# Kernel optimization log

Hardware: AMD Instinct MI355X
Metric: run time of the kernel (lower is better)

## Reference

```python
import jax, jax.numpy as jnp
import numpy as np


def setup_inputs() -> dict:
    key = jax.random.key(0)
    k1, k2 = jax.random.split(key)
    n, c, H, W = 8, 16, 512, 512
    pred = jax.random.normal(k1, (n, c, H, W), dtype=jnp.float32)
    target = jax.random.randint(k2, (n, H, W), 0, c, dtype=jnp.int64)
    weights = jnp.ones((n, 1, H, W), dtype=jnp.float32)  # ignored by the module
    return {"pred": pred, "target": target, "weights": weights}


def reference(pred, target, weights):
    # pred: [n,c,H,W] logits; target: [n,H,W] int class ids; weights arg is ignored
    n, c, H, W = pred.shape
    # Global (whole-batch) per-class pixel counts -> inverse-frequency weights.
    counts = jnp.zeros((c,), dtype=pred.dtype).at[target.reshape(-1)].add(1.0)
    w_class = jnp.where(counts > 0, 1.0 / (counts * c), 0.0)  # [c]
    w = w_class[target]  # [n,H,W] per-pixel weight (constant w.r.t. pred)
    # log-softmax gathered at target class per pixel
    logp = jax.nn.log_softmax(pred, axis=1)  # [n,c,H,W]
    lp_t = jnp.take_along_axis(logp, target[:, None, :, :], axis=1)[:, 0]  # [n,H,W]
    num = (lp_t * w).reshape(n, -1).sum(axis=1)  # [n]
    den = w.reshape(n, -1).sum(axis=1)           # [n]
    return -(num / den).mean()
```

## Files before the change

### kernel.cpp

```cpp
#include <hip/hip_runtime.h>

#define NIMG 8
#define NCLS 16
#define HW      262144
#define PXB     2048
#define NBLK    1024
#define GROUPS  2

__global__ __launch_bounds__(256) void dwce_main(const float* __restrict__ pred,
                                                 const int* __restrict__ tgt,
                                                 float* __restrict__ partials) {
    __shared__ float s_bin[32];
    const int tid = threadIdx.x;
    if (tid < 32) s_bin[tid] = 0.0f;
    __syncthreads();

    const int b = blockIdx.x;
    const long long px0 = (long long)b * PXB;
    const int n_img = (int)(px0 >> 18);
    const int hw0   = (int)(px0 & (HW - 1));
    const float* base = pred + (size_t)n_img * NCLS * HW + hw0;

    const int w    = tid >> 6;
    const int lane = tid & 63;
    int idx[GROUPS];
#pragma unroll
    for (int g = 0; g < GROUPS; ++g)
        idx[g] = w * (GROUPS * 256) + g * 256 + lane * 4;

    int4 t[GROUPS];
#pragma unroll
    for (int g = 0; g < GROUPS; ++g)
        t[g] = *(const int4*)(tgt + px0 + idx[g]);

    float4 m[GROUPS], s[GROUPS], xt[GROUPS];
#pragma unroll
    for (int g = 0; g < GROUPS; ++g) {
        m[g]  = make_float4(-3.0e38f, -3.0e38f, -3.0e38f, -3.0e38f);
        s[g]  = make_float4(0.f, 0.f, 0.f, 0.f);
        xt[g] = make_float4(0.f, 0.f, 0.f, 0.f);
    }

#pragma unroll 2
    for (int c = 0; c < NCLS; ++c) {
        const float* cb = base + (size_t)c * HW;
#pragma unroll
        for (int g = 0; g < GROUPS; ++g) {
            const float4 v = *(const float4*)(cb + idx[g]);
            float4 mn;
            mn.x = fmaxf(m[g].x, v.x);
            mn.y = fmaxf(m[g].y, v.y);
            mn.z = fmaxf(m[g].z, v.z);
            mn.w = fmaxf(m[g].w, v.w);
            s[g].x = s[g].x * __expf(m[g].x - mn.x) + __expf(v.x - mn.x);
            s[g].y = s[g].y * __expf(m[g].y - mn.y) + __expf(v.y - mn.y);
            s[g].z = s[g].z * __expf(m[g].z - mn.z) + __expf(v.z - mn.z);
            s[g].w = s[g].w * __expf(m[g].w - mn.w) + __expf(v.w - mn.w);
            m[g] = mn;
            if (t[g].x == c) xt[g].x = v.x;
            if (t[g].y == c) xt[g].y = v.y;
            if (t[g].z == c) xt[g].z = v.z;
            if (t[g].w == c) xt[g].w = v.w;
        }
    }

#pragma unroll
    for (int g = 0; g < GROUPS; ++g) {
        const float lp0 = xt[g].x - (m[g].x + __logf(s[g].x));
        const float lp1 = xt[g].y - (m[g].y + __logf(s[g].y));
        const float lp2 = xt[g].z - (m[g].z + __logf(s[g].z));
        const float lp3 = xt[g].w - (m[g].w + __logf(s[g].w));
        atomicAdd(&s_bin[t[g].x], lp0);
        atomicAdd(&s_bin[t[g].y], lp1);
        atomicAdd(&s_bin[t[g].z], lp2);
        atomicAdd(&s_bin[t[g].w], lp3);
        atomicAdd(&s_bin[16 + t[g].x], 1.0f);
        atomicAdd(&s_bin[16 + t[g].y], 1.0f);
        atomicAdd(&s_bin[16 + t[g].z], 1.0f);
        atomicAdd(&s_bin[16 + t[g].w], 1.0f);
    }

    __syncthreads();
    if (tid < 32)
        partials[(size_t)tid * NBLK + b] = s_bin[tid];
}

__global__ __launch_bounds__(256) void dwce_final(const float* __restrict__ ws,
                                                  float* __restrict__ out) {
    __shared__ float tot[32][NIMG];
    __shared__ float wcl[NCLS];
    __shared__ float ratio[NIMG];
    const int tid = threadIdx.x;
    const int c = tid >> 3;
    const int n = tid & 7;

    const float4* p = (const float4*)(ws + (size_t)c * NBLK + n * 128);
    float4 a = make_float4(0.f, 0.f, 0.f, 0.f);
#pragma unroll 8
    for (int k = 0; k < 32; ++k) {
        float4 q = p[k];
        a.x += q.x; a.y += q.y; a.z += q.z; a.w += q.w;
    }
    tot[c][n] = (a.x + a.y) + (a.z + a.w);
    __syncthreads();

    if (tid < NCLS) {
        float g = 0.f;
#pragma unroll
        for (int i = 0; i < NIMG; ++i) g += tot[NCLS + tid][i];
        wcl[tid] = (g > 0.f) ? 1.0f / (g * (float)NCLS) : 0.0f;
    }
    __syncthreads();
    if (tid < NIMG) {
        float num = 0.f, den = 0.f;
#pragma unroll
        for (int c2 = 0; c2 < NCLS; ++c2) {
            num += tot[c2][tid] * wcl[c2];
            den += tot[NCLS + c2][tid] * wcl[c2];
        }
        ratio[tid] = num / den;
    }
    __syncthreads();
    if (tid == 0) {
        float r = 0.f;
#pragma unroll
        for (int i = 0; i < NIMG; ++i) r += ratio[i];
        out[0] = -r * (1.0f / (float)NIMG);
    }
}

extern "C" void kernel_launch(void* const* d_in, const int* in_sizes, int n_in,
                              void* d_out, int out_size, void* d_ws, size_t ws_size,
                              hipStream_t stream) {
    const float* pred = (const float*)d_in[0];
    const int*   tgt  = (const int*)d_in[1];
    float* out = (float*)d_out;
    float* ws  = (float*)d_ws;

    dwce_main<<<NBLK, 256, 0, stream>>>(pred, tgt, ws);
    dwce_final<<<1, 256, 0, stream>>>(ws, out);
}
```

Baseline: 223.0 us.

## Stage logits in LDS via global_load_lds and use two-pass softmax

```diff
diff --git a/kernel.cpp b/kernel.cpp
--- a/kernel.cpp
+++ b/kernel.cpp
@@ -1,19 +1,26 @@
 #include <hip/hip_runtime.h>
+#include <stdint.h>
 
 #define NIMG 8
 #define NCLS 16
-#define HW      262144
-#define PXB     2048
-#define NBLK    1024
-#define GROUPS  2
+#define HW   262144
+#define PXB  1024
+#define NBLK 2048
+
+__device__ __forceinline__ void g2lds16(const float* g, float* l) {
+    __builtin_amdgcn_global_load_lds(
+        (const __attribute__((address_space(1))) unsigned int*)g,
+        (__attribute__((address_space(3))) unsigned int*)l,
+        16, 0, 0);
+}
 
 __global__ __launch_bounds__(256) void dwce_main(const float* __restrict__ pred,
                                                  const int* __restrict__ tgt,
                                                  float* __restrict__ partials) {
+    __shared__ float tile[NCLS * PXB];
     __shared__ float s_bin[32];
     const int tid = threadIdx.x;
     if (tid < 32) s_bin[tid] = 0.0f;
-    __syncthreads();
 
     const int b = blockIdx.x;
     const long long px0 = (long long)b * PXB;
@@ -23,62 +30,56 @@
 
     const int w    = tid >> 6;
     const int lane = tid & 63;
-    int idx[GROUPS];
+    const int woff = w * 256 + lane * 4;
+
 #pragma unroll
-    for (int g = 0; g < GROUPS; ++g)
-        idx[g] = w * (GROUPS * 256) + g * 256 + lane * 4;
+    for (int c = 0; c < NCLS; ++c)
+        g2lds16(base + (size_t)c * HW + woff, &tile[c * PXB + woff]);
 
-    int4 t[GROUPS];
+    const int4 t4 = *(const int4*)(tgt + px0 + tid * 4);
+
+    __syncthreads();
+
+    const int p = tid * 4;
+
+    float4 m  = make_float4(-3.0e38f, -3.0e38f, -3.0e38f, -3.0e38f);
+    float4 xt = make_float4(0.f, 0.f, 0.f, 0.f);
 #pragma unroll
-    for (int g = 0; g < GROUPS; ++g)
-        t[g] = *(const int4*)(tgt + px0 + idx[g]);
-
-    float4 m[GROUPS], s[GROUPS], xt[GROUPS];
-#pragma unroll
-    for (int g = 0; g < GROUPS; ++g) {
-        m[g]  = make_float4(-3.0e38f, -3.0e38f, -3.0e38f, -3.0e38f);
-        s[g]  = make_float4(0.f, 0.f, 0.f, 0.f);
-        xt[g] = make_float4(0.f, 0.f, 0.f, 0.f);
+    for (int c = 0; c < NCLS; ++c) {
+        const float4 v = *(const float4*)&tile[c * PXB + p];
+        m.x = fmaxf(m.x, v.x);
+        m.y = fmaxf(m.y, v.y);
+        m.z = fmaxf(m.z, v.z);
+        m.w = fmaxf(m.w, v.w);
+        if (t4.x == c) xt.x = v.x;
+        if (t4.y == c) xt.y = v.y;
+        if (t4.z == c) xt.z = v.z;
+        if (t4.w == c) xt.w = v.w;
     }
 
-#pragma unroll 2
+    float4 s = make_float4(0.f, 0.f, 0.f, 0.f);
+#pragma unroll
     for (int c = 0; c < NCLS; ++c) {
-        const float* cb = base + (size_t)c * HW;
-#pragma unroll
-        for (int g = 0; g < GROUPS; ++g) {
-            const float4 v = *(const float4*)(cb + idx[g]);
-            float4 mn;
-            mn.x = fmaxf(m[g].x, v.x);
-            mn.y = fmaxf(m[g].y, v.y);
-            mn.z = fmaxf(m[g].z, v.z);
-            mn.w = fmaxf(m[g].w, v.w);
-            s[g].x = s[g].x * __expf(m[g].x - mn.x) + __expf(v.x - mn.x);
-            s[g].y = s[g].y * __expf(m[g].y - mn.y) + __expf(v.y - mn.y);
-            s[g].z = s[g].z * __expf(m[g].z - mn.z) + __expf(v.z - mn.z);
-            s[g].w = s[g].w * __expf(m[g].w - mn.w) + __expf(v.w - mn.w);
-            m[g] = mn;
-            if (t[g].x == c) xt[g].x = v.x;
-            if (t[g].y == c) xt[g].y = v.y;
-            if (t[g].z == c) xt[g].z = v.z;
-            if (t[g].w == c) xt[g].w = v.w;
-        }
+        const float4 v = *(const float4*)&tile[c * PXB + p];
+        s.x += __expf(v.x - m.x);
+        s.y += __expf(v.y - m.y);
+        s.z += __expf(v.z - m.z);
+        s.w += __expf(v.w - m.w);
     }
 
-#pragma unroll
-    for (int g = 0; g < GROUPS; ++g) {
-        const float lp0 = xt[g].x - (m[g].x + __logf(s[g].x));
-        const float lp1 = xt[g].y - (m[g].y + __logf(s[g].y));
-        const float lp2 = xt[g].z - (m[g].z + __logf(s[g].z));
-        const float lp3 = xt[g].w - (m[g].w + __logf(s[g].w));
-        atomicAdd(&s_bin[t[g].x], lp0);
-        atomicAdd(&s_bin[t[g].y], lp1);
-        atomicAdd(&s_bin[t[g].z], lp2);
-        atomicAdd(&s_bin[t[g].w], lp3);
-        atomicAdd(&s_bin[16 + t[g].x], 1.0f);
-        atomicAdd(&s_bin[16 + t[g].y], 1.0f);
-        atomicAdd(&s_bin[16 + t[g].z], 1.0f);
-        atomicAdd(&s_bin[16 + t[g].w], 1.0f);
-    }
+    const float lp0 = xt.x - (m.x + __logf(s.x));
+    const float lp1 = xt.y - (m.y + __logf(s.y));
+    const float lp2 = xt.z - (m.z + __logf(s.z));
+    const float lp3 = xt.w - (m.w + __logf(s.w));
+
+    atomicAdd(&s_bin[t4.x], lp0);
+    atomicAdd(&s_bin[t4.y], lp1);
+    atomicAdd(&s_bin[t4.z], lp2);
+    atomicAdd(&s_bin[t4.w], lp3);
+    atomicAdd(&s_bin[16 + t4.x], 1.0f);
+    atomicAdd(&s_bin[16 + t4.y], 1.0f);
+    atomicAdd(&s_bin[16 + t4.z], 1.0f);
+    atomicAdd(&s_bin[16 + t4.w], 1.0f);
 
     __syncthreads();
     if (tid < 32)
@@ -94,10 +95,10 @@
     const int c = tid >> 3;
     const int n = tid & 7;
 
-    const float4* p = (const float4*)(ws + (size_t)c * NBLK + n * 128);
+    const float4* p = (const float4*)(ws + (size_t)c * NBLK + n * 256);
     float4 a = make_float4(0.f, 0.f, 0.f, 0.f);
 #pragma unroll 8
-    for (int k = 0; k < 32; ++k) {
+    for (int k = 0; k < 64; ++k) {
         float4 q = p[k];
         a.x += q.x; a.y += q.y; a.z += q.z; a.w += q.w;
     }
```

New measurement: 206.8 us. 7.3% less time.
